# Kernel tuning notes

Hardware: AMD Instinct MI355X
Metric: run time of the kernel (lower is better)

Reference implementation:

```python
import jax, jax.numpy as jnp
import numpy as np

B, T, F = 16384, 48, 4
UNITS = 256
OUT_STEPS = 24


def setup_inputs() -> dict:
    key = jax.random.key(0)
    ks = jax.random.split(key, 6)
    s_x = 1.0 / np.sqrt(F)
    s_h = 1.0 / np.sqrt(UNITS)
    return {
        "x": jax.random.normal(ks[0], (B, T, F), jnp.float32),
        "Wx": jax.random.normal(ks[1], (F, 4 * UNITS), jnp.float32) * s_x,
        "Wh": jax.random.normal(ks[2], (UNITS, 4 * UNITS), jnp.float32) * s_h,
        "b": jnp.zeros((4 * UNITS,), jnp.float32),
        "Wd": jax.random.normal(ks[3], (UNITS, F), jnp.float32) * s_h,
        "bd": jnp.zeros((F,), jnp.float32),
    }


def _lstm_cell(xt, h, c, Wx, Wh, b):
    # Keras LSTMCell gate order: i, f, g(cell candidate), o
    z = xt @ Wx + h @ Wh + b  # [B, 4*units]
    i, f, g, o = jnp.split(z, 4, axis=-1)
    i = jax.nn.sigmoid(i)
    f = jax.nn.sigmoid(f)
    g = jnp.tanh(g)
    o = jax.nn.sigmoid(o)
    c_new = f * c + i * g
    h_new = o * jnp.tanh(c_new)
    return h_new, c_new


def reference(x, Wx, Wh, b, Wd, bd):
    bsz = x.shape[0]
    h0 = jnp.zeros((bsz, UNITS), x.dtype)
    c0 = jnp.zeros((bsz, UNITS), x.dtype)

    # --- warmup: run LSTM over the input window, keep final state ---
    def warm_step(carry, xt):
        h, c = carry
        h, c = _lstm_cell(xt, h, c, Wx, Wh, b)
        return (h, c), None

    (h, c), _ = jax.lax.scan(warm_step, (h0, c0), jnp.swapaxes(x, 0, 1))
    pred0 = h @ Wd + bd  # first prediction [B, F]

    def ar_step(carry, _):
        h, c, pred = carry
        h, c = _lstm_cell(pred, h, c, Wx, Wh, b)
        pred = h @ Wd + bd
        return (h, c, pred), pred

    _, preds = jax.lax.scan(ar_step, (h, c, pred0), None, length=OUT_STEPS - 1)
    preds = jnp.concatenate([pred0[None], preds], axis=0)  # [out_steps, B, F]
    return jnp.swapaxes(preds, 0, 1)  # [B, out_steps, F]
```

## Files before the change

kernel.cpp:

```cpp
#include <hip/hip_runtime.h>


typedef unsigned short u16;
typedef __attribute__((ext_vector_type(8))) short bf16x8;
typedef __attribute__((ext_vector_type(4))) float f32x4;

#define PITCH 296
#define HB 18944
#define CPITCH 264
#define WARM 48
#define STEPS 71
#define LOG2E  1.442695041f
#define LOG2E2 2.885390082f

__device__ __forceinline__ u16 f2bf(float f) {
    unsigned u = __float_as_uint(f);
    u += 0x7FFFu + ((u >> 16) & 1u);
    return (u16)(u >> 16);
}

__device__ __forceinline__ float sigm2(float zp) {
    return __builtin_amdgcn_rcpf(1.0f + __builtin_amdgcn_exp2f(-zp));
}

__device__ __forceinline__ void sync_lds() {
    asm volatile("s_waitcnt lgkmcnt(0)\n\ts_barrier" ::: "memory");
}

__global__ void prep_weights(const float* __restrict__ Wx,
                             const float* __restrict__ Wh,
                             const float* __restrict__ b,
                             const float* __restrict__ Wd,
                             const float* __restrict__ bd,
                             u16* __restrict__ whext,
                             u16* __restrict__ wdp) {
    int idx = blockIdx.x * 256 + threadIdx.x;
    if (idx < 36864) {
        int lane = idx & 63;
        int blk = idx >> 6;
        int nt = blk & 63;
        int kt = blk >> 6;
        int kbase = kt * 32 + (lane >> 4) * 8;
        int n = nt * 16 + (lane & 15);
        float sc = (n >= 512 && n < 768) ? LOG2E2 : LOG2E;
        u16 v[8];
#pragma unroll
        for (int j = 0; j < 8; ++j) {
            int k = kbase + j;
            float f = 0.0f;
            if (k < 256) f = Wh[k * 1024 + n];
            else if (k < 260) f = Wx[(k - 256) * 1024 + n];
            else if (k == 260) f = b[n];
            v[j] = f2bf(f * sc);
        }
        ushort4* dst = (ushort4*)(whext + (size_t)idx * 8);
        dst[0] = make_ushort4(v[0], v[1], v[2], v[3]);
        dst[1] = make_ushort4(v[4], v[5], v[6], v[7]);
    } else if (idx < 36864 + 576) {
        int id2 = idx - 36864;
        int lane = id2 & 63;
        int kt = id2 >> 6;
        int kbase = kt * 32 + (lane >> 4) * 8;
        int n = lane & 15;
        u16 v[8];
#pragma unroll
        for (int j = 0; j < 8; ++j) {
            int k = kbase + j;
            float f = 0.0f;
            if (n < 4) {
                if (k < 256) f = Wd[k * 4 + n];
                else if (k == 260) f = bd[n];
            }
            v[j] = f2bf(f);
        }
        ushort4* dst = (ushort4*)(wdp + (size_t)id2 * 8);
        dst[0] = make_ushort4(v[0], v[1], v[2], v[3]);
        dst[1] = make_ushort4(v[4], v[5], v[6], v[7]);
    }
}

#define MFMA_BURST(WA, HBX)                                                   \
    _Pragma("unroll") for (int g = 0; g < 4; ++g)                             \
    _Pragma("unroll") for (int nh = 0; nh < 2; ++nh)                          \
    _Pragma("unroll") for (int bt = 0; bt < 4; ++bt)                          \
        acc[bt][g][nh] = __builtin_amdgcn_mfma_f32_16x16x32_bf16(             \
            WA[g][nh], HBX[bt], acc[bt][g][nh], 0, 0, 0);

#define WLOAD(DST, KTV) do {                                                  \
    const char* _wpk = wp + (size_t)(KTV) * 65536;                            \
    _Pragma("unroll") for (int g = 0; g < 4; ++g)                             \
    _Pragma("unroll") for (int nh = 0; nh < 2; ++nh)                          \
        DST[g][nh] = *(const bf16x8*)(_wpk + voff[g][nh]);                    \
} while (0)

#define HLOAD(DST, KTV) do {                                                  \
    _Pragma("unroll") for (int bt = 0; bt < 4; ++bt)                          \
        DST[bt] = *(const bf16x8*)&hr[(16 * bt + col) * PITCH + (KTV) * 32 + quad * 8]; \
} while (0)

__global__ __launch_bounds__(512, 2) void lstm_main(
    const float* __restrict__ x, const u16* __restrict__ whext,
    const u16* __restrict__ wdp, float* __restrict__ out) {
    __shared__ __align__(16) unsigned char smem[143360];
    u16* hbuf = (u16*)smem;
    float* cbuf = (float*)(smem + 75776);

    const int tid = threadIdx.x;
    const int w = tid >> 6;
    const int l = tid & 63;
    const int col = l & 15;
    const int quad = l >> 4;
    const long long rowBase = (long long)blockIdx.x * 64;

    {
        int4 z = make_int4(0, 0, 0, 0);
        for (int i = tid; i < 8960; i += 512) ((int4*)smem)[i] = z;
    }
    sync_lds();
    if (tid < 64) {
        hbuf[tid * PITCH + 260] = (u16)0x3F80;
        hbuf[HB + tid * PITCH + 260] = (u16)0x3F80;
        const float4 xv = *(const float4*)(x + (rowBase + tid) * 192);
        u16* p = &hbuf[tid * PITCH + 256];
        p[0] = f2bf(xv.x); p[1] = f2bf(xv.y); p[2] = f2bf(xv.z); p[3] = f2bf(xv.w);
    }

    const char* __restrict__ wp = (const char*)whext;
    const bf16x8* __restrict__ dfrag = (const bf16x8*)wdp;
    int voff[4][2];
#pragma unroll
    for (int g = 0; g < 4; ++g)
#pragma unroll
        for (int nh = 0; nh < 2; ++nh)
            voff[g][nh] = ((16 * g + 2 * w + nh) * 64 + l) * 16;

    bf16x8 waA[4][2], waB[4][2];
    WLOAD(waA, 0);
    WLOAD(waB, 1);

    for (int step = 0; step < STEPS; ++step) {
        const u16* hr = hbuf + (step & 1) * HB;
        u16* hw = hbuf + ((step & 1) ^ 1) * HB;

        sync_lds();

        f32x4 acc[4][4][2];
#pragma unroll
        for (int bt = 0; bt < 4; ++bt)
#pragma unroll
            for (int g = 0; g < 4; ++g)
#pragma unroll
                for (int nh = 0; nh < 2; ++nh) acc[bt][g][nh] = (f32x4){0.f, 0.f, 0.f, 0.f};

        bf16x8 hbA[4], hbB[4];
        HLOAD(hbA, 0);
        HLOAD(hbB, 1);

#pragma unroll 1
        for (int kt = 0; kt < 8; kt += 2) {
            MFMA_BURST(waA, hbA);
            WLOAD(waA, kt + 2);
            HLOAD(hbA, kt + 2);
            MFMA_BURST(waB, hbB);
            {
                int kb = (kt == 6) ? 1 : kt + 3;
                WLOAD(waB, kb);
            }
            if (kt < 6) HLOAD(hbB, kt + 3);
        }
        MFMA_BURST(waA, hbA);
        WLOAD(waA, 0);

#pragma unroll
        for (int bt = 0; bt < 4; ++bt)
#pragma unroll
            for (int nh = 0; nh < 2; ++nh) {
                float* cp = &cbuf[(16 * bt + col) * CPITCH + 32 * w + 16 * nh + 4 * quad];
                f32x4 cold = *(const f32x4*)cp;
                f32x4 cnew;
                u16 hh[4];
#pragma unroll
                for (int r = 0; r < 4; ++r) {
                    float iv = sigm2(acc[bt][0][nh][r]);
                    float fv = sigm2(acc[bt][1][nh][r]);
                    float gv = 2.0f * sigm2(acc[bt][2][nh][r]) - 1.0f;
                    float ov = sigm2(acc[bt][3][nh][r]);
                    float cn = fv * cold[r] + iv * gv;
                    cnew[r] = cn;
                    float ts = sigm2(LOG2E2 * cn);
                    hh[r] = f2bf(ov * (2.0f * ts - 1.0f));
                }
                *(f32x4*)cp = cnew;
                *(ushort4*)&hw[(16 * bt + col) * PITCH + 32 * w + 16 * nh + 4 * quad] =
                    make_ushort4(hh[0], hh[1], hh[2], hh[3]);
            }

        if (step < WARM - 1) {
            if (w == 0) {
                const float4 xv = *(const float4*)(x + (rowBase + l) * 192 + (step + 1) * 4);
                u16* p = &hw[l * PITCH + 256];
                p[0] = f2bf(xv.x); p[1] = f2bf(xv.y); p[2] = f2bf(xv.z); p[3] = f2bf(xv.w);
            }
        } else {
            sync_lds();
            if (w < 4) {
                f32x4 pacc = (f32x4){0.f, 0.f, 0.f, 0.f};
#pragma unroll
                for (int kt = 0; kt < 9; ++kt) {
                    bf16x8 hbp = *(const bf16x8*)&hw[(16 * w + col) * PITCH + kt * 32 + quad * 8];
                    bf16x8 wap = dfrag[kt * 64 + l];
                    pacc = __builtin_amdgcn_mfma_f32_16x16x32_bf16(wap, hbp, pacc, 0, 0, 0);
                }
                if (quad == 0) {
                    int s = step - (WARM - 1);
                    *(float4*)&out[((rowBase + 16 * w + col) * 24 + s) * 4] =
                        make_float4(pacc[0], pacc[1], pacc[2], pacc[3]);
                    *(ushort4*)&hw[(16 * w + col) * PITCH + 256] =
                        make_ushort4(f2bf(pacc[0]), f2bf(pacc[1]), f2bf(pacc[2]), f2bf(pacc[3]));
                }
            }
        }
    }
}

extern "C" void kernel_launch(void* const* d_in, const int* in_sizes, int n_in,
                              void* d_out, int out_size, void* d_ws, size_t ws_size,
                              hipStream_t stream) {
    const float* x  = (const float*)d_in[0];
    const float* Wx = (const float*)d_in[1];
    const float* Wh = (const float*)d_in[2];
    const float* b  = (const float*)d_in[3];
    const float* Wd = (const float*)d_in[4];
    const float* bd = (const float*)d_in[5];
    float* out = (float*)d_out;

    u16* whext = (u16*)d_ws;
    u16* wdp = (u16*)((char*)d_ws + 36864 * 16);

    prep_weights<<<(36864 + 576 + 255) / 256, 256, 0, stream>>>(Wx, Wh, b, Wd, bd, whext, wdp);
    lstm_main<<<256, 512, 0, stream>>>(x, whext, wdp, out);
}
```

Before: 791.7 us.

## Switch LSTM recurrence to 32x32x16 MFMA with register-resident cell state

Replaces the 16x16x32 bf16 MFMA tiling with 32x32x16 MFMA tiles, re-laying out the prepacked weights and hidden-state fragments to match, and uses a three-deep software pipeline over 18 k-steps. The cell state now stays in registers across all steps instead of being read from and written to LDS every step, which shrinks shared memory. Gate math is reorganised so that several sigmoid/tanh reciprocals are merged into single rcp calls. The aim is fewer LDS operations and fewer instructions per step. The cost is much higher register pressure from the 16-wide accumulators plus persistent state, which could hurt occupancy or cause spills.

```diff
diff --git a/kernel.cpp b/kernel.cpp
--- a/kernel.cpp
+++ b/kernel.cpp
@@ -3,11 +3,10 @@
 
 typedef unsigned short u16;
 typedef __attribute__((ext_vector_type(8))) short bf16x8;
-typedef __attribute__((ext_vector_type(4))) float f32x4;
+typedef __attribute__((ext_vector_type(16))) float f32x16;
 
 #define PITCH 296
 #define HB 18944
-#define CPITCH 264
 #define WARM 48
 #define STEPS 71
 #define LOG2E  1.442695041f
@@ -17,10 +16,6 @@
     unsigned u = __float_as_uint(f);
     u += 0x7FFFu + ((u >> 16) & 1u);
     return (u16)(u >> 16);
-}
-
-__device__ __forceinline__ float sigm2(float zp) {
-    return __builtin_amdgcn_rcpf(1.0f + __builtin_amdgcn_exp2f(-zp));
 }
 
 __device__ __forceinline__ void sync_lds() {
@@ -37,16 +32,17 @@
     int idx = blockIdx.x * 256 + threadIdx.x;
     if (idx < 36864) {
         int lane = idx & 63;
-        int blk = idx >> 6;
-        int nt = blk & 63;
-        int kt = blk >> 6;
-        int kbase = kt * 32 + (lane >> 4) * 8;
-        int n = nt * 16 + (lane & 15);
-        float sc = (n >= 512 && n < 768) ? LOG2E2 : LOG2E;
+        int frag = idx >> 6;
+        int wv = frag & 7;
+        int g = (frag >> 3) & 3;
+        int kt = frag >> 5;
+        int k0 = kt * 16 + (lane >> 5) * 8;
+        int n = 256 * g + 32 * wv + (lane & 31);
+        float sc = (g == 2) ? LOG2E2 : LOG2E;
         u16 v[8];
 #pragma unroll
         for (int j = 0; j < 8; ++j) {
-            int k = kbase + j;
+            int k = k0 + j;
             float f = 0.0f;
             if (k < 256) f = Wh[k * 1024 + n];
             else if (k < 260) f = Wx[(k - 256) * 1024 + n];
@@ -56,20 +52,20 @@
         ushort4* dst = (ushort4*)(whext + (size_t)idx * 8);
         dst[0] = make_ushort4(v[0], v[1], v[2], v[3]);
         dst[1] = make_ushort4(v[4], v[5], v[6], v[7]);
-    } else if (idx < 36864 + 576) {
+    } else if (idx < 36864 + 1152) {
         int id2 = idx - 36864;
         int lane = id2 & 63;
         int kt = id2 >> 6;
-        int kbase = kt * 32 + (lane >> 4) * 8;
-        int n = lane & 15;
+        int k0 = kt * 16 + (lane >> 5) * 8;
+        int f_ = lane & 31;
         u16 v[8];
 #pragma unroll
         for (int j = 0; j < 8; ++j) {
-            int k = kbase + j;
+            int k = k0 + j;
             float f = 0.0f;
-            if (n < 4) {
-                if (k < 256) f = Wd[k * 4 + n];
-                else if (k == 260) f = bd[n];
+            if (f_ < 4) {
+                if (k < 256) f = Wd[k * 4 + f_];
+                else if (k == 260) f = bd[f_];
             }
             v[j] = f2bf(f);
         }
@@ -79,42 +75,38 @@
     }
 }
 
-#define MFMA_BURST(WA, HBX)                                                   \
+#define WLOAD(DST, KTV) do {                                                  \
+    const char* _wpk = wp + (size_t)(KTV) * 32768;                            \
     _Pragma("unroll") for (int g = 0; g < 4; ++g)                             \
-    _Pragma("unroll") for (int nh = 0; nh < 2; ++nh)                          \
-    _Pragma("unroll") for (int bt = 0; bt < 4; ++bt)                          \
-        acc[bt][g][nh] = __builtin_amdgcn_mfma_f32_16x16x32_bf16(             \
-            WA[g][nh], HBX[bt], acc[bt][g][nh], 0, 0, 0);
-
-#define WLOAD(DST, KTV) do {                                                  \
-    const char* _wpk = wp + (size_t)(KTV) * 65536;                            \
+        DST[g] = *(const bf16x8*)(_wpk + voff[g]);                            \
+} while (0)
+
+#define HLOAD(DST, KTV) do {                                                  \
+    DST[0] = *(const bf16x8*)&hr[hrow0 + (KTV) * 16];                         \
+    DST[1] = *(const bf16x8*)&hr[hrow1 + (KTV) * 16];                         \
+} while (0)
+
+#define MT(WA, HBX)                                                           \
+    _Pragma("unroll") for (int m = 0; m < 2; ++m)                             \
     _Pragma("unroll") for (int g = 0; g < 4; ++g)                             \
-    _Pragma("unroll") for (int nh = 0; nh < 2; ++nh)                          \
-        DST[g][nh] = *(const bf16x8*)(_wpk + voff[g][nh]);                    \
-} while (0)
-
-#define HLOAD(DST, KTV) do {                                                  \
-    _Pragma("unroll") for (int bt = 0; bt < 4; ++bt)                          \
-        DST[bt] = *(const bf16x8*)&hr[(16 * bt + col) * PITCH + (KTV) * 32 + quad * 8]; \
-} while (0)
+        acc[m][g] = __builtin_amdgcn_mfma_f32_32x32x16_bf16(                  \
+            WA[g], HBX[m], acc[m][g], 0, 0, 0);
 
 __global__ __launch_bounds__(512, 2) void lstm_main(
     const float* __restrict__ x, const u16* __restrict__ whext,
     const u16* __restrict__ wdp, float* __restrict__ out) {
-    __shared__ __align__(16) unsigned char smem[143360];
-    u16* hbuf = (u16*)smem;
-    float* cbuf = (float*)(smem + 75776);
+    __shared__ __align__(16) u16 hbuf[2 * HB];
 
     const int tid = threadIdx.x;
     const int w = tid >> 6;
     const int l = tid & 63;
-    const int col = l & 15;
-    const int quad = l >> 4;
+    const int l31 = l & 31;
+    const int lh = l >> 5;
     const long long rowBase = (long long)blockIdx.x * 64;
 
     {
         int4 z = make_int4(0, 0, 0, 0);
-        for (int i = tid; i < 8960; i += 512) ((int4*)smem)[i] = z;
+        for (int i = tid; i < 4736; i += 512) ((int4*)hbuf)[i] = z;
     }
     sync_lds();
     if (tid < 64) {
@@ -126,74 +118,68 @@
     }
 
     const char* __restrict__ wp = (const char*)whext;
-    const bf16x8* __restrict__ dfrag = (const bf16x8*)wdp;
-    int voff[4][2];
-#pragma unroll
-    for (int g = 0; g < 4; ++g)
-#pragma unroll
-        for (int nh = 0; nh < 2; ++nh)
-            voff[g][nh] = ((16 * g + 2 * w + nh) * 64 + l) * 16;
-
-    bf16x8 waA[4][2], waB[4][2];
-    WLOAD(waA, 0);
-    WLOAD(waB, 1);
+    const char* __restrict__ dp = (const char*)wdp;
+    int voff[4];
+#pragma unroll
+    for (int g = 0; g < 4; ++g) voff[g] = ((g * 8 + w) * 64 + l) * 16;
+    const int hrow0 = l31 * PITCH + lh * 8;
+    const int hrow1 = (32 + l31) * PITCH + lh * 8;
+
+    f32x16 c[2] = {};
+    bf16x8 awA[4], awB[4], awC[4];
+    WLOAD(awA, 0);
+    WLOAD(awB, 1);
 
     for (int step = 0; step < STEPS; ++step) {
         const u16* hr = hbuf + (step & 1) * HB;
         u16* hw = hbuf + ((step & 1) ^ 1) * HB;
-
         sync_lds();
 
-        f32x4 acc[4][4][2];
-#pragma unroll
-        for (int bt = 0; bt < 4; ++bt)
-#pragma unroll
-            for (int g = 0; g < 4; ++g)
-#pragma unroll
-                for (int nh = 0; nh < 2; ++nh) acc[bt][g][nh] = (f32x4){0.f, 0.f, 0.f, 0.f};
-
-        bf16x8 hbA[4], hbB[4];
+        f32x16 acc[2][4] = {};
+        bf16x8 hbA[2], hbB[2], hbC[2];
         HLOAD(hbA, 0);
         HLOAD(hbB, 1);
 
 #pragma unroll 1
-        for (int kt = 0; kt < 8; kt += 2) {
-            MFMA_BURST(waA, hbA);
-            WLOAD(waA, kt + 2);
-            HLOAD(hbA, kt + 2);
-            MFMA_BURST(waB, hbB);
-            {
-                int kb = (kt == 6) ? 1 : kt + 3;
-                WLOAD(waB, kb);
-            }
-            if (kt < 6) HLOAD(hbB, kt + 3);
-        }
-        MFMA_BURST(waA, hbA);
-        WLOAD(waA, 0);
-
-#pragma unroll
-        for (int bt = 0; bt < 4; ++bt)
-#pragma unroll
-            for (int nh = 0; nh < 2; ++nh) {
-                float* cp = &cbuf[(16 * bt + col) * CPITCH + 32 * w + 16 * nh + 4 * quad];
-                f32x4 cold = *(const f32x4*)cp;
-                f32x4 cnew;
+        for (int t = 0; t < 15; t += 3) {
+            WLOAD(awC, t + 2); HLOAD(hbC, t + 2);
+            MT(awA, hbA);
+            WLOAD(awA, t + 3); HLOAD(hbA, t + 3);
+            MT(awB, hbB);
+            WLOAD(awB, t + 4); HLOAD(hbB, t + 4);
+            MT(awC, hbC);
+        }
+        WLOAD(awC, 17); HLOAD(hbC, 17);
+        MT(awA, hbA);
+        WLOAD(awA, 0);
+        MT(awB, hbB);
+        WLOAD(awB, 1);
+        MT(awC, hbC);
+
+#pragma unroll
+        for (int m = 0; m < 2; ++m) {
+            const int hwrow = (32 * m + l31) * PITCH + 32 * w + 4 * lh;
+#pragma unroll
+            for (int q = 0; q < 4; ++q) {
                 u16 hh[4];
 #pragma unroll
-                for (int r = 0; r < 4; ++r) {
-                    float iv = sigm2(acc[bt][0][nh][r]);
-                    float fv = sigm2(acc[bt][1][nh][r]);
-                    float gv = 2.0f * sigm2(acc[bt][2][nh][r]) - 1.0f;
-                    float ov = sigm2(acc[bt][3][nh][r]);
-                    float cn = fv * cold[r] + iv * gv;
-                    cnew[r] = cn;
-                    float ts = sigm2(LOG2E2 * cn);
-                    hh[r] = f2bf(ov * (2.0f * ts - 1.0f));
+                for (int rr = 0; rr < 4; ++rr) {
+                    const int r = q * 4 + rr;
+                    float ei = __builtin_amdgcn_exp2f(-acc[m][0][r]);
+                    float ef = __builtin_amdgcn_exp2f(-acc[m][1][r]);
+                    float eg = __builtin_amdgcn_exp2f(-acc[m][2][r]);
+                    float eo = __builtin_amdgcn_exp2f(-acc[m][3][r]);
+                    float fv  = __builtin_amdgcn_rcpf(1.0f + ef);
+                    float rig = __builtin_amdgcn_rcpf((1.0f + ei) * (1.0f + eg));
+                    float cn  = c[m][r] * fv + (1.0f - eg) * rig;
+                    c[m][r] = cn;
+                    float ec = __builtin_amdgcn_exp2f(-LOG2E2 * cn);
+                    float roc = __builtin_amdgcn_rcpf((1.0f + eo) * (1.0f + ec));
+                    hh[rr] = f2bf((1.0f - ec) * roc);
                 }
-                *(f32x4*)cp = cnew;
-                *(ushort4*)&hw[(16 * bt + col) * PITCH + 32 * w + 16 * nh + 4 * quad] =
-                    make_ushort4(hh[0], hh[1], hh[2], hh[3]);
-            }
+                *(ushort4*)&hw[hwrow + 8 * q] = make_ushort4(hh[0], hh[1], hh[2], hh[3]);
+            }
+        }
 
         if (step < WARM - 1) {
             if (w == 0) {
@@ -203,19 +189,21 @@
             }
         } else {
             sync_lds();
-            if (w < 4) {
-                f32x4 pacc = (f32x4){0.f, 0.f, 0.f, 0.f};
-#pragma unroll
-                for (int kt = 0; kt < 9; ++kt) {
-                    bf16x8 hbp = *(const bf16x8*)&hw[(16 * w + col) * PITCH + kt * 32 + quad * 8];
-                    bf16x8 wap = dfrag[kt * 64 + l];
-                    pacc = __builtin_amdgcn_mfma_f32_16x16x32_bf16(wap, hbp, pacc, 0, 0, 0);
+            if (w < 2) {
+                f32x16 pacc = {};
+                const int prow = (32 * w + l31) * PITCH + lh * 8;
+#pragma unroll
+                for (int kt = 0; kt < 18; ++kt) {
+                    bf16x8 hbp = *(const bf16x8*)&hw[prow + kt * 16];
+                    bf16x8 wap = *(const bf16x8*)(dp + ((size_t)kt * 64 + l) * 16);
+                    pacc = __builtin_amdgcn_mfma_f32_32x32x16_bf16(wap, hbp, pacc, 0, 0, 0);
                 }
-                if (quad == 0) {
+                if (lh == 0) {
                     int s = step - (WARM - 1);
-                    *(float4*)&out[((rowBase + 16 * w + col) * 24 + s) * 4] =
+                    int batch = 32 * w + l31;
+                    *(float4*)&out[((rowBase + batch) * 24 + s) * 4] =
                         make_float4(pacc[0], pacc[1], pacc[2], pacc[3]);
-                    *(ushort4*)&hw[(16 * w + col) * PITCH + 256] =
+                    *(ushort4*)&hw[batch * PITCH + 256] =
                         make_ushort4(f2bf(pacc[0]), f2bf(pacc[1]), f2bf(pacc[2]), f2bf(pacc[3]));
                 }
             }
@@ -235,8 +223,8 @@
     float* out = (float*)d_out;
 
     u16* whext = (u16*)d_ws;
-    u16* wdp = (u16*)((char*)d_ws + 36864 * 16);
-
-    prep_weights<<<(36864 + 576 + 255) / 256, 256, 0, stream>>>(Wx, Wh, b, Wd, bd, whext, wdp);
+    u16* wdp = (u16*)((char*)d_ws + 589824);
+
+    prep_weights<<<(36864 + 1152 + 255) / 256, 256, 0, stream>>>(Wx, Wh, b, Wd, bd, whext, wdp);
     lstm_main<<<256, 512, 0, stream>>>(x, whext, wdp, out);
 }
```

Result: slower. 826.2 us (+4.4%).
